# Optimization experiments

Hardware: AMD Instinct MI355X
Metric: run time of the kernel (lower is better)

## Reference

```python
import jax, jax.numpy as jnp
import numpy as np

B, T, F, H = 64, 128, 1024, 1024
FORGET_BIAS = 1.0  # TF BasicLSTMCell default


def setup_inputs() -> dict:
    key = jax.random.key(0)
    k1, k2 = jax.random.split(key, 2)
    x = jax.random.normal(k1, (B, T, F), dtype=jnp.float32)
    # single fused kernel weight [(F+H), 4H], TF gate order: i, j, f, o
    W = jax.random.uniform(k2, (F + H, 4 * H), dtype=jnp.float32, minval=-0.1, maxval=0.1)
    b = jnp.zeros((4 * H,), dtype=jnp.float32)
    return {"x": x, "W": W, "b": b}


def reference(x, W, b):
    # BasicLSTMCell unrolled over time (return_last=False, return_seq_2d=False)
    batch, n_steps, n_feat = x.shape
    n_hidden = W.shape[0] - n_feat

    def step(carry, xt):
        c, h = carry
        z = jnp.concatenate([xt, h], axis=1) @ W + b  # [B, 4H]
        i, j, f, o = jnp.split(z, 4, axis=1)
        c_new = c * jax.nn.sigmoid(f + FORGET_BIAS) + jax.nn.sigmoid(i) * jnp.tanh(j)
        h_new = jnp.tanh(c_new) * jax.nn.sigmoid(o)
        return (c_new, h_new), h_new

    c0 = jnp.zeros((batch, n_hidden), x.dtype)
    h0 = jnp.zeros((batch, n_hidden), x.dtype)
    _, hs = jax.lax.scan(step, (c0, h0), jnp.swapaxes(x, 0, 1))  # [T, B, H]
    return jnp.swapaxes(hs, 0, 1)  # [B, T, H]
```

## Files before the change

kernel.cpp:

```cpp
#include <hip/hip_runtime.h>
#include <hip/hip_bf16.h>

typedef unsigned short u16;
typedef unsigned int u32;
typedef unsigned long long u64;
typedef __bf16 bf16x8 __attribute__((ext_vector_type(8)));
typedef float f32x4 __attribute__((ext_vector_type(4)));

#define NB 64
#define NT 128
#define NF 1024
#define NH 1024
#define NK 2048
#define NG 4096
#define NBH (NB * NH)

#define FSTR 16

#define W_LDS_BYTES 131072
#define ZSX_BYTES (2 * 2 * 64 * 17 * 4)
#define ZSH_BYTES (2 * 64 * 17 * 4)
#define SMEM_BYTES (W_LDS_BYTES + ZSX_BYTES + ZSH_BYTES + 64)

__device__ __forceinline__ u16 f2bf(float f) {
  unsigned u = __builtin_bit_cast(unsigned, f);
  u = (u + 0x7FFFu + ((u >> 16) & 1u)) >> 16;
  return (u16)u;
}
__device__ __forceinline__ float bf2f(u16 v) {
  unsigned u = ((unsigned)v) << 16;
  return __builtin_bit_cast(float, u);
}

__global__ __launch_bounds__(256) void lstm_cvt_x(const float* __restrict__ x,
                                                  u16* __restrict__ xb) {
  int i = (blockIdx.x * 256 + threadIdx.x) * 4;
  float4 v = *reinterpret_cast<const float4*>(x + i);
  ushort4 o;
  o.x = f2bf(v.x); o.y = f2bf(v.y); o.z = f2bf(v.z); o.w = f2bf(v.w);
  *reinterpret_cast<ushort4*>(xb + i) = o;
}

__global__ __launch_bounds__(256) void lstm_prep_w(const float* __restrict__ W,
                                                   u16* __restrict__ wt_blk) {
  __shared__ float tile[32][33];
  int n0 = blockIdx.x * 32;
  int k0 = blockIdx.y * 32;
  int tc = threadIdx.x & 31;
  int tr = threadIdx.x >> 5;
#pragma unroll
  for (int i = 0; i < 4; ++i) {
    int k = tr + i * 8;
    tile[k][tc] = W[(size_t)(k0 + k) * NG + n0 + tc];
  }
  __syncthreads();
#pragma unroll
  for (int i = 0; i < 4; ++i) {
    int n = n0 + tr + i * 8;
    float wv = tile[tc][tr + i * 8];
    int k = k0 + tc;
    int g = n >> 10, col = n & 1023;
    int b = col >> 2, brow = g * 4 + (col & 3);
    int kh = k >> 10, ch = (k & 1023) >> 5;
    int slot = (k >> 3) & 3, elem = k & 7;
    size_t base = (size_t)b * 65536 + (size_t)(kh * 32 + ch) * 512
                + (size_t)(slot * 16 + brow) * 8 + elem;
    u16 hi = f2bf(wv);
    wt_blk[base] = hi;
    wt_blk[base + 32768] = f2bf(wv - bf2f(hi));
  }
}

__device__ __forceinline__ void mfma_pass(const u16* __restrict__ a0, size_t rstride,
                                          const u16* __restrict__ Wl, int khalf,
                                          int kq, int lane, f32x4 acc[4]) {
  bf16x8 pf[4], qf[4];
#pragma unroll
  for (int i = 0; i < 4; ++i)
    pf[i] = *reinterpret_cast<const bf16x8*>(a0 + (size_t)i * 16 * rstride);
#pragma unroll
  for (int cc = 0; cc < 8; ++cc) {
    if (cc < 7) {
#pragma unroll
      for (int i = 0; i < 4; ++i)
        qf[i] = *reinterpret_cast<const bf16x8*>(a0 + (size_t)i * 16 * rstride + (cc + 1) * 32);
    }
    const int ch = kq * 8 + cc;
    const bf16x8 wh = *reinterpret_cast<const bf16x8*>(
        Wl + (size_t)(khalf * 32 + ch) * 512 + lane * 8);
    const bf16x8 wl2 = *reinterpret_cast<const bf16x8*>(
        Wl + (size_t)(64 + khalf * 32 + ch) * 512 + lane * 8);
#pragma unroll
    for (int i = 0; i < 4; ++i)
      acc[i] = __builtin_amdgcn_mfma_f32_16x16x32_bf16(pf[i], wh, acc[i], 0, 0, 0);
#pragma unroll
    for (int i = 0; i < 4; ++i)
      acc[i] = __builtin_amdgcn_mfma_f32_16x16x32_bf16(pf[i], wl2, acc[i], 0, 0, 0);
#pragma unroll
    for (int i = 0; i < 4; ++i) pf[i] = qf[i];
  }
}

__global__ __launch_bounds__(512) void lstm_persist(
    const u16* __restrict__ xb, u16* __restrict__ hseq,
    const u16* __restrict__ wt_blk, const float* __restrict__ bias,
    float* __restrict__ out, u32* __restrict__ flags,
    float* __restrict__ zo) {
  extern __shared__ char smem[];
  u16* Wl = (u16*)smem;
  float (*zsx)[2][64][17] = (float(*)[2][64][17])(smem + W_LDS_BYTES);
  float (*zsh)[64][17] = (float(*)[64][17])(smem + W_LDS_BYTES + ZSX_BYTES);
  volatile u32* hsflag = (volatile u32*)(smem + W_LDS_BYTES + ZSX_BYTES + ZSH_BYTES);

  const int b = blockIdx.x;
  const int tid = threadIdx.x;
  const int lane = tid & 63;
  const int w = tid >> 6;
  const bool is_x = (w < 4);
  const int kq = w & 3;

  {
    const u16* src = wt_blk + (size_t)b * 65536;
#pragma unroll
    for (int it = 0; it < 16; ++it) {
      uint4 v = *reinterpret_cast<const uint4*>(src + (size_t)it * 4096 + tid * 8);
      *reinterpret_cast<uint4*>(Wl + (size_t)it * 4096 + tid * 8) = v;
    }
  }
  for (int i = tid; i < 2 * 64 * 17; i += 512) ((float*)zsh)[i] = 0.f;
  if (tid == 0) hsflag[0] = 0u;

  const int arow = lane & 15;
  const int kfr = 8 * (lane >> 4);
  const int kbase = kq * 256 + kfr;
  const int zn = lane & 15;
  const int mg = (lane >> 4) * 4;

  const int prow = tid >> 1;
  const int pc = (tid & 1) * 2;
  const int gc0 = b * 4 + pc;
  float bz[2][4];
  float creg[2] = {0.f, 0.f};
  if (tid < 128) {
#pragma unroll
    for (int j = 0; j < 2; ++j) {
      bz[j][0] = bias[gc0 + j];
      bz[j][1] = bias[NH + gc0 + j];
      bz[j][2] = bias[2 * NH + gc0 + j];
      bz[j][3] = bias[3 * NH + gc0 + j];
    }
  }
  __syncthreads();

  {
    f32x4 acc[4] = {};
    if (is_x) {
      const u16* a0 = xb + ((size_t)arow * NT + 0) * NF + kbase;
      mfma_pass(a0, (size_t)NT * NF, Wl, 0, kq, lane, acc);
      if (w < 2) {
#pragma unroll
        for (int i = 0; i < 4; ++i)
#pragma unroll
          for (int r = 0; r < 4; ++r) zsx[0][w][i * 16 + mg + r][zn] = acc[i][r];
      }
    }
    __syncthreads();
    if (is_x && w >= 2) {
#pragma unroll
      for (int i = 0; i < 4; ++i)
#pragma unroll
        for (int r = 0; r < 4; ++r) zsx[0][w - 2][i * 16 + mg + r][zn] += acc[i][r];
    }
    __syncthreads();
  }

#pragma unroll 1
  for (int t = 0; t < NT; ++t) {
    const int cb = t & 1;
    const int nb = (t + 1) & 1;
    f32x4 acc[4] = {};

    if (is_x) {
      if (t < NT - 1) {
        const u16* a0 = xb + ((size_t)arow * NT + (t + 1)) * NF + kbase;
        mfma_pass(a0, (size_t)NT * NF, Wl, 0, kq, lane, acc);
      }
    } else {
      if (t > 0) {
        const u32* fp = flags + ((size_t)t * 256 + kq * 64 + lane) * FSTR;
        u32 v = __hip_atomic_load(fp, __ATOMIC_RELAXED, __HIP_MEMORY_SCOPE_AGENT);
        while (!__all(v != 0)) {
          __builtin_amdgcn_s_sleep(1);
          v = __hip_atomic_load(fp, __ATOMIC_RELAXED, __HIP_MEMORY_SCOPE_AGENT);
        }

        const u64* hb = reinterpret_cast<const u64*>(hseq) + (size_t)t * (256 * 64);
        const int sbase = kq * 64 + 2 * (lane >> 4);
        u64 plo[4], phi[4], qlo[4], qhi[4];
#pragma unroll
        for (int i = 0; i < 4; ++i) {
          plo[i] = hb[(size_t)sbase * 64 + arow + 16 * i];
          phi[i] = hb[(size_t)(sbase + 1) * 64 + arow + 16 * i];
        }
        __builtin_amdgcn_s_setprio(1);
#pragma unroll
        for (int cc = 0; cc < 8; ++cc) {
          if (cc < 7) {
            const int s = sbase + (cc + 1) * 8;
#pragma unroll
            for (int i = 0; i < 4; ++i) {
              qlo[i] = hb[(size_t)s * 64 + arow + 16 * i];
              qhi[i] = hb[(size_t)(s + 1) * 64 + arow + 16 * i];
            }
          }
          const int ch = kq * 8 + cc;
          const bf16x8 wh = *reinterpret_cast<const bf16x8*>(
              Wl + (size_t)(32 + ch) * 512 + lane * 8);
          const bf16x8 wlo = *reinterpret_cast<const bf16x8*>(
              Wl + (size_t)(96 + ch) * 512 + lane * 8);
#pragma unroll
          for (int i = 0; i < 4; ++i) {
            union HU { u64 q[2]; bf16x8 f; } u;
            u.q[0] = plo[i];
            u.q[1] = phi[i];
            acc[i] = __builtin_amdgcn_mfma_f32_16x16x32_bf16(u.f, wh, acc[i], 0, 0, 0);
            acc[i] = __builtin_amdgcn_mfma_f32_16x16x32_bf16(u.f, wlo, acc[i], 0, 0, 0);
          }
#pragma unroll
          for (int i = 0; i < 4; ++i) { plo[i] = qlo[i]; phi[i] = qhi[i]; }
        }
        __builtin_amdgcn_s_setprio(0);
      }
    }

    if (is_x) {
      if (w < 2 && t < NT - 1) {
#pragma unroll
        for (int i = 0; i < 4; ++i)
#pragma unroll
          for (int r = 0; r < 4; ++r) zsx[nb][w][i * 16 + mg + r][zn] = acc[i][r];
      }
    } else {
      if (w < 6 && t > 0) {
#pragma unroll
        for (int i = 0; i < 4; ++i)
#pragma unroll
          for (int r = 0; r < 4; ++r) zsh[w - 4][i * 16 + mg + r][zn] = acc[i][r];
      }
    }
    __syncthreads();
    if (is_x) {
      if (w >= 2 && t < NT - 1) {
#pragma unroll
        for (int i = 0; i < 4; ++i)
#pragma unroll
          for (int r = 0; r < 4; ++r) zsx[nb][w - 2][i * 16 + mg + r][zn] += acc[i][r];
      }
    } else {
      if (w >= 6 && t > 0) {
#pragma unroll
        for (int i = 0; i < 4; ++i)
#pragma unroll
          for (int r = 0; r < 4; ++r) zsh[w - 6][i * 16 + mg + r][zn] += acc[i][r];
      }
    }
    __syncthreads();

    if (tid < 128) {
      float hn[2];
#pragma unroll
      for (int jj = 0; jj < 2; ++jj) {
        const int col = pc + jj;
        const float zi = zsx[cb][0][prow][col]      + zsx[cb][1][prow][col]      + zsh[0][prow][col]      + zsh[1][prow][col]      + bz[jj][0];
        const float zj = zsx[cb][0][prow][4 + col]  + zsx[cb][1][prow][4 + col]  + zsh[0][prow][4 + col]  + zsh[1][prow][4 + col]  + bz[jj][1];
        const float zf = zsx[cb][0][prow][8 + col]  + zsx[cb][1][prow][8 + col]  + zsh[0][prow][8 + col]  + zsh[1][prow][8 + col]  + bz[jj][2];
        const float zo4 = zsx[cb][0][prow][12 + col] + zsx[cb][1][prow][12 + col] + zsh[0][prow][12 + col] + zsh[1][prow][12 + col] + bz[jj][3];
        const float si = 1.f / (1.f + __expf(-zi));
        const float tj = tanhf(zj);
        const float sf = 1.f / (1.f + __expf(-(zf + 1.0f)));
        const float so = 1.f / (1.f + __expf(-zo4));
        const float cn = creg[jj] * sf + si * tj;
        hn[jj] = tanhf(cn) * so;
        creg[jj] = cn;
      }
      if (t < NT - 1) {
        u32 hv = (u32)f2bf(hn[0]) | ((u32)f2bf(hn[1]) << 16);
        u32* hp = reinterpret_cast<u32*>(hseq)
                + ((size_t)(t + 1) * 256 + b) * 128 + prow * 2 + (pc >> 1);
        __hip_atomic_store(hp, hv, __ATOMIC_RELAXED, __HIP_MEMORY_SCOPE_AGENT);
        asm volatile("s_waitcnt vmcnt(0)" ::: "memory");
        if (tid == 64) hsflag[0] = (u32)(t + 1);
        if (tid == 0) {
          while (hsflag[0] != (u32)(t + 1)) {}
          __hip_atomic_store(&flags[((size_t)(t + 1) * 256 + b) * FSTR], 1u,
                             __ATOMIC_RELAXED, __HIP_MEMORY_SCOPE_AGENT);
        }
      }
#pragma unroll
      for (int jj = 0; jj < 2; ++jj) {
        __hip_atomic_store(
            reinterpret_cast<u32*>(zo + ((size_t)t * NH + gc0 + jj) * NB + prow),
            __builtin_bit_cast(u32, hn[jj]),
            __ATOMIC_RELAXED, __HIP_MEMORY_SCOPE_AGENT);
      }
    }
  }

  __syncthreads();
  asm volatile("s_waitcnt vmcnt(0)" ::: "memory");
  if (tid == 0)
    __hip_atomic_store(&flags[(size_t)b * FSTR], 1u, __ATOMIC_RELAXED,
                       __HIP_MEMORY_SCOPE_AGENT);
  if (w == 0) {
    bool ok;
    do {
      u32 v0 = __hip_atomic_load(flags + (size_t)(lane * 4 + 0) * FSTR, __ATOMIC_RELAXED, __HIP_MEMORY_SCOPE_AGENT);
      u32 v1 = __hip_atomic_load(flags + (size_t)(lane * 4 + 1) * FSTR, __ATOMIC_RELAXED, __HIP_MEMORY_SCOPE_AGENT);
      u32 v2 = __hip_atomic_load(flags + (size_t)(lane * 4 + 2) * FSTR, __ATOMIC_RELAXED, __HIP_MEMORY_SCOPE_AGENT);
      u32 v3 = __hip_atomic_load(flags + (size_t)(lane * 4 + 3) * FSTR, __ATOMIC_RELAXED, __HIP_MEMORY_SCOPE_AGENT);
      ok = ((v0 & v1 & v2 & v3) == 1u);
      if (!__all(ok)) __builtin_amdgcn_s_sleep(1);
    } while (!__all(ok));
  }
  __syncthreads();

  {
    const int ts = b >> 1;
    const int r0 = (b & 1) * 32;
    float* T = (float*)smem;
#pragma unroll 4
    for (int it = 0; it < 16; ++it) {
      int flat = it * 512 + tid;
      int c = flat >> 3;
      int q = flat & 7;
      const u64* p = reinterpret_cast<const u64*>(
          zo + ((size_t)ts * NH + c) * NB + r0 + q * 4);
      u64 lo = __hip_atomic_load(p + 0, __ATOMIC_RELAXED, __HIP_MEMORY_SCOPE_AGENT);
      u64 hi = __hip_atomic_load(p + 1, __ATOMIC_RELAXED, __HIP_MEMORY_SCOPE_AGENT);
      T[(q * 4 + 0) * 1028 + c] = __builtin_bit_cast(float, (u32)lo);
      T[(q * 4 + 1) * 1028 + c] = __builtin_bit_cast(float, (u32)(lo >> 32));
      T[(q * 4 + 2) * 1028 + c] = __builtin_bit_cast(float, (u32)hi);
      T[(q * 4 + 3) * 1028 + c] = __builtin_bit_cast(float, (u32)(hi >> 32));
    }
    __syncthreads();
#pragma unroll 4
    for (int it = 0; it < 16; ++it) {
      int flat = it * 512 + tid;
      int r = flat >> 8;
      int c4 = flat & 255;
      float4 v;
      v.x = T[r * 1028 + c4 * 4 + 0];
      v.y = T[r * 1028 + c4 * 4 + 1];
      v.z = T[r * 1028 + c4 * 4 + 2];
      v.w = T[r * 1028 + c4 * 4 + 3];
      *reinterpret_cast<float4*>(
          out + ((size_t)(r0 + r) * NT + ts) * NH + c4 * 4) = v;
    }
  }
}

extern "C" void kernel_launch(void* const* d_in, const int* in_sizes, int n_in,
                              void* d_out, int out_size, void* d_ws, size_t ws_size,
                              hipStream_t stream) {
  const float* x = (const float*)d_in[0];
  const float* W = (const float*)d_in[1];
  const float* bias = (const float*)d_in[2];
  float* out = (float*)d_out;

  char* ws = (char*)d_ws;
  u16* xb = (u16*)(ws);
  u16* wt_blk = (u16*)(ws + 16777216);
  u16* hseq = (u16*)(ws + 50331648);
  u32* flags = (u32*)(ws + 67108864);
  float* zo = (float*)(ws + 69206016);

  hipMemsetAsync(hseq, 0, 256 * 512, stream);
  hipMemsetAsync(flags, 0, (size_t)NT * 256 * FSTR * 4, stream);

  lstm_cvt_x<<<(NB * NT * NF) / (256 * 4), 256, 0, stream>>>(x, xb);
  lstm_prep_w<<<dim3(NG / 32, NK / 32), 256, 0, stream>>>(W, wt_blk);

  hipFuncSetAttribute((const void*)lstm_persist,
                      hipFuncAttributeMaxDynamicSharedMemorySize, SMEM_BYTES);

  void* args[] = {(void*)&xb, (void*)&hseq, (void*)&wt_blk, (void*)&bias,
                  (void*)&out, (void*)&flags, (void*)&zo};
  hipLaunchCooperativeKernel((void*)lstm_persist, dim3(256), dim3(512), args,
                             SMEM_BYTES, stream);
}
```

Before: 1.038 ms.

## Replace per-step block barriers with LDS flag-based warp specialization

Replaces the two __syncthreads per timestep with fine-grained LDS counters using release/acquire spin-waits. X-projection waves now run up to two steps ahead of the recurrent waves, and the pointwise work moves onto two of the h waves. The aim is to take the x-side GEMM off the critical serial path and remove block-wide barrier stalls. In exchange it adds spin-waiting in LDS, and there is a risk of ordering bugs in the double-buffered zsx reuse.

```diff
diff --git a/kernel.cpp b/kernel.cpp
--- a/kernel.cpp
+++ b/kernel.cpp
@@ -20,7 +20,18 @@
 #define W_LDS_BYTES 131072
 #define ZSX_BYTES (2 * 2 * 64 * 17 * 4)
 #define ZSH_BYTES (2 * 64 * 17 * 4)
-#define SMEM_BYTES (W_LDS_BYTES + ZSX_BYTES + ZSH_BYTES + 64)
+#define ST_BYTES 64
+#define SMEM_BYTES (W_LDS_BYTES + ZSX_BYTES + ZSH_BYTES + ST_BYTES)
+
+__device__ __forceinline__ void st_rel(u32* p, u32 v) {
+  __hip_atomic_store(p, v, __ATOMIC_RELEASE, __HIP_MEMORY_SCOPE_WORKGROUP);
+}
+__device__ __forceinline__ u32 ld_acq(u32* p) {
+  return __hip_atomic_load(p, __ATOMIC_ACQUIRE, __HIP_MEMORY_SCOPE_WORKGROUP);
+}
+__device__ __forceinline__ void spin_ge(u32* p, u32 v) {
+  while (ld_acq(p) < v) {}
+}
 
 __device__ __forceinline__ u16 f2bf(float f) {
   unsigned u = __builtin_bit_cast(unsigned, f);
@@ -110,14 +121,15 @@
   u16* Wl = (u16*)smem;
   float (*zsx)[2][64][17] = (float(*)[2][64][17])(smem + W_LDS_BYTES);
   float (*zsh)[64][17] = (float(*)[64][17])(smem + W_LDS_BYTES + ZSX_BYTES);
-  volatile u32* hsflag = (volatile u32*)(smem + W_LDS_BYTES + ZSX_BYTES + ZSH_BYTES);
+  u32* st = (u32*)(smem + W_LDS_BYTES + ZSX_BYTES + ZSH_BYTES);
 
   const int b = blockIdx.x;
   const int tid = threadIdx.x;
   const int lane = tid & 63;
-  const int w = tid >> 6;
-  const bool is_x = (w < 4);
-  const int kq = w & 3;
+  const int wv_ = tid >> 6;
+  const bool is_x = (wv_ < 4);
+  const int kq = wv_ & 3;
+  const int hq = wv_ - 4;
 
   {
     const u16* src = wt_blk + (size_t)b * 65536;
@@ -128,7 +140,7 @@
     }
   }
   for (int i = tid; i < 2 * 64 * 17; i += 512) ((float*)zsh)[i] = 0.f;
-  if (tid == 0) hsflag[0] = 0u;
+  if (tid < 16) st[tid] = 0u;
 
   const int arow = lane & 15;
   const int kfr = 8 * (lane >> 4);
@@ -136,12 +148,13 @@
   const int zn = lane & 15;
   const int mg = (lane >> 4) * 4;
 
-  const int prow = tid >> 1;
-  const int pc = (tid & 1) * 2;
+  const int idx = hq * 64 + lane;
+  const int prow = (idx & 127) >> 1;
+  const int pc = (idx & 1) * 2;
   const int gc0 = b * 4 + pc;
   float bz[2][4];
   float creg[2] = {0.f, 0.f};
-  if (tid < 128) {
+  if (!is_x && hq < 2) {
 #pragma unroll
     for (int j = 0; j < 2; ++j) {
       bz[j][0] = bias[gc0 + j];
@@ -152,40 +165,36 @@
   }
   __syncthreads();
 
-  {
-    f32x4 acc[4] = {};
-    if (is_x) {
-      const u16* a0 = xb + ((size_t)arow * NT + 0) * NF + kbase;
+  if (is_x) {
+#pragma unroll 1
+    for (int t = 0; t < NT; ++t) {
+      if (t >= 2) {
+        spin_ge(&st[8], (u32)(t - 1));
+        spin_ge(&st[9], (u32)(t - 1));
+      }
+      f32x4 acc[4] = {};
+      const u16* a0 = xb + ((size_t)arow * NT + t) * NF + kbase;
       mfma_pass(a0, (size_t)NT * NF, Wl, 0, kq, lane, acc);
-      if (w < 2) {
+      const int buf = t & 1;
+      if (kq < 2) {
 #pragma unroll
         for (int i = 0; i < 4; ++i)
 #pragma unroll
-          for (int r = 0; r < 4; ++r) zsx[0][w][i * 16 + mg + r][zn] = acc[i][r];
+          for (int r = 0; r < 4; ++r) zsx[buf][kq][i * 16 + mg + r][zn] = acc[i][r];
+        st_rel(&st[kq], (u32)(t + 1));
+      } else {
+        spin_ge(&st[kq - 2], (u32)(t + 1));
+#pragma unroll
+        for (int i = 0; i < 4; ++i)
+#pragma unroll
+          for (int r = 0; r < 4; ++r) zsx[buf][kq - 2][i * 16 + mg + r][zn] += acc[i][r];
+        st_rel(&st[kq], (u32)(t + 1));
       }
     }
-    __syncthreads();
-    if (is_x && w >= 2) {
-#pragma unroll
-      for (int i = 0; i < 4; ++i)
-#pragma unroll
-        for (int r = 0; r < 4; ++r) zsx[0][w - 2][i * 16 + mg + r][zn] += acc[i][r];
-    }
-    __syncthreads();
-  }
-
+  } else {
 #pragma unroll 1
-  for (int t = 0; t < NT; ++t) {
-    const int cb = t & 1;
-    const int nb = (t + 1) & 1;
-    f32x4 acc[4] = {};
-
-    if (is_x) {
-      if (t < NT - 1) {
-        const u16* a0 = xb + ((size_t)arow * NT + (t + 1)) * NF + kbase;
-        mfma_pass(a0, (size_t)NT * NF, Wl, 0, kq, lane, acc);
-      }
-    } else {
+    for (int t = 0; t < NT; ++t) {
+      f32x4 acc[4] = {};
       if (t > 0) {
         const u32* fp = flags + ((size_t)t * 256 + kq * 64 + lane) * FSTR;
         u32 v = __hip_atomic_load(fp, __ATOMIC_RELAXED, __HIP_MEMORY_SCOPE_AGENT);
@@ -193,7 +202,6 @@
           __builtin_amdgcn_s_sleep(1);
           v = __hip_atomic_load(fp, __ATOMIC_RELAXED, __HIP_MEMORY_SCOPE_AGENT);
         }
-
         const u64* hb = reinterpret_cast<const u64*>(hseq) + (size_t)t * (256 * 64);
         const int sbase = kq * 64 + 2 * (lane >> 4);
         u64 plo[4], phi[4], qlo[4], qhi[4];
@@ -231,77 +239,68 @@
         }
         __builtin_amdgcn_s_setprio(0);
       }
-    }
-
-    if (is_x) {
-      if (w < 2 && t < NT - 1) {
-#pragma unroll
-        for (int i = 0; i < 4; ++i)
-#pragma unroll
-          for (int r = 0; r < 4; ++r) zsx[nb][w][i * 16 + mg + r][zn] = acc[i][r];
-      }
-    } else {
-      if (w < 6 && t > 0) {
-#pragma unroll
-        for (int i = 0; i < 4; ++i)
-#pragma unroll
-          for (int r = 0; r < 4; ++r) zsh[w - 4][i * 16 + mg + r][zn] = acc[i][r];
-      }
-    }
-    __syncthreads();
-    if (is_x) {
-      if (w >= 2 && t < NT - 1) {
-#pragma unroll
-        for (int i = 0; i < 4; ++i)
-#pragma unroll
-          for (int r = 0; r < 4; ++r) zsx[nb][w - 2][i * 16 + mg + r][zn] += acc[i][r];
-      }
-    } else {
-      if (w >= 6 && t > 0) {
-#pragma unroll
-        for (int i = 0; i < 4; ++i)
-#pragma unroll
-          for (int r = 0; r < 4; ++r) zsh[w - 6][i * 16 + mg + r][zn] += acc[i][r];
-      }
-    }
-    __syncthreads();
-
-    if (tid < 128) {
-      float hn[2];
-#pragma unroll
-      for (int jj = 0; jj < 2; ++jj) {
-        const int col = pc + jj;
-        const float zi = zsx[cb][0][prow][col]      + zsx[cb][1][prow][col]      + zsh[0][prow][col]      + zsh[1][prow][col]      + bz[jj][0];
-        const float zj = zsx[cb][0][prow][4 + col]  + zsx[cb][1][prow][4 + col]  + zsh[0][prow][4 + col]  + zsh[1][prow][4 + col]  + bz[jj][1];
-        const float zf = zsx[cb][0][prow][8 + col]  + zsx[cb][1][prow][8 + col]  + zsh[0][prow][8 + col]  + zsh[1][prow][8 + col]  + bz[jj][2];
-        const float zo4 = zsx[cb][0][prow][12 + col] + zsx[cb][1][prow][12 + col] + zsh[0][prow][12 + col] + zsh[1][prow][12 + col] + bz[jj][3];
-        const float si = 1.f / (1.f + __expf(-zi));
-        const float tj = tanhf(zj);
-        const float sf = 1.f / (1.f + __expf(-(zf + 1.0f)));
-        const float so = 1.f / (1.f + __expf(-zo4));
-        const float cn = creg[jj] * sf + si * tj;
-        hn[jj] = tanhf(cn) * so;
-        creg[jj] = cn;
-      }
-      if (t < NT - 1) {
-        u32 hv = (u32)f2bf(hn[0]) | ((u32)f2bf(hn[1]) << 16);
-        u32* hp = reinterpret_cast<u32*>(hseq)
-                + ((size_t)(t + 1) * 256 + b) * 128 + prow * 2 + (pc >> 1);
-        __hip_atomic_store(hp, hv, __ATOMIC_RELAXED, __HIP_MEMORY_SCOPE_AGENT);
-        asm volatile("s_waitcnt vmcnt(0)" ::: "memory");
-        if (tid == 64) hsflag[0] = (u32)(t + 1);
-        if (tid == 0) {
-          while (hsflag[0] != (u32)(t + 1)) {}
-          __hip_atomic_store(&flags[((size_t)(t + 1) * 256 + b) * FSTR], 1u,
-                             __ATOMIC_RELAXED, __HIP_MEMORY_SCOPE_AGENT);
-        }
-      }
-#pragma unroll
-      for (int jj = 0; jj < 2; ++jj) {
-        __hip_atomic_store(
-            reinterpret_cast<u32*>(zo + ((size_t)t * NH + gc0 + jj) * NB + prow),
-            __builtin_bit_cast(u32, hn[jj]),
-            __ATOMIC_RELAXED, __HIP_MEMORY_SCOPE_AGENT);
+
+      if (hq < 2) {
+        spin_ge(&st[8 + (1 - hq)], (u32)t);
+        if (t > 0) {
+#pragma unroll
+          for (int i = 0; i < 4; ++i)
+#pragma unroll
+            for (int r = 0; r < 4; ++r) zsh[hq][i * 16 + mg + r][zn] = acc[i][r];
+        }
+        st_rel(&st[4 + hq], (u32)(t + 1));
+
+        spin_ge(&st[6], (u32)(t + 1));
+        spin_ge(&st[7], (u32)(t + 1));
+        spin_ge(&st[2], (u32)(t + 1));
+        spin_ge(&st[3], (u32)(t + 1));
+        const int cb = t & 1;
+        float hn[2];
+#pragma unroll
+        for (int jj = 0; jj < 2; ++jj) {
+          const int col = pc + jj;
+          const float zi = zsx[cb][0][prow][col]      + zsx[cb][1][prow][col]      + zsh[0][prow][col]      + zsh[1][prow][col]      + bz[jj][0];
+          const float zj = zsx[cb][0][prow][4 + col]  + zsx[cb][1][prow][4 + col]  + zsh[0][prow][4 + col]  + zsh[1][prow][4 + col]  + bz[jj][1];
+          const float zf = zsx[cb][0][prow][8 + col]  + zsx[cb][1][prow][8 + col]  + zsh[0][prow][8 + col]  + zsh[1][prow][8 + col]  + bz[jj][2];
+          const float zo4 = zsx[cb][0][prow][12 + col] + zsx[cb][1][prow][12 + col] + zsh[0][prow][12 + col] + zsh[1][prow][12 + col] + bz[jj][3];
+          const float si = 1.f / (1.f + __expf(-zi));
+          const float tj = tanhf(zj);
+          const float sf = 1.f / (1.f + __expf(-(zf + 1.0f)));
+          const float so = 1.f / (1.f + __expf(-zo4));
+          const float cn = creg[jj] * sf + si * tj;
+          hn[jj] = tanhf(cn) * so;
+          creg[jj] = cn;
+        }
+        if (t < NT - 1) {
+          u32 hv = (u32)f2bf(hn[0]) | ((u32)f2bf(hn[1]) << 16);
+          u32* hp = reinterpret_cast<u32*>(hseq)
+                  + ((size_t)(t + 1) * 256 + b) * 128 + prow * 2 + (pc >> 1);
+          __hip_atomic_store(hp, hv, __ATOMIC_RELAXED, __HIP_MEMORY_SCOPE_AGENT);
+          asm volatile("s_waitcnt vmcnt(0)" ::: "memory");
+        }
+        st_rel(&st[8 + hq], (u32)(t + 1));
+        if (hq == 0 && t < NT - 1) {
+          spin_ge(&st[9], (u32)(t + 1));
+          if (lane == 0)
+            __hip_atomic_store(&flags[((size_t)(t + 1) * 256 + b) * FSTR], 1u,
+                               __ATOMIC_RELAXED, __HIP_MEMORY_SCOPE_AGENT);
+        }
+#pragma unroll
+        for (int jj = 0; jj < 2; ++jj) {
+          __hip_atomic_store(
+              reinterpret_cast<u32*>(zo + ((size_t)t * NH + gc0 + jj) * NB + prow),
+              __builtin_bit_cast(u32, hn[jj]),
+              __ATOMIC_RELAXED, __HIP_MEMORY_SCOPE_AGENT);
+        }
+      } else {
+        spin_ge(&st[4 + (hq - 2)], (u32)(t + 1));
+        if (t > 0) {
+#pragma unroll
+          for (int i = 0; i < 4; ++i)
+#pragma unroll
+            for (int r = 0; r < 4; ++r) zsh[hq - 2][i * 16 + mg + r][zn] += acc[i][r];
+        }
+        st_rel(&st[4 + hq], (u32)(t + 1));
       }
     }
   }
@@ -311,7 +310,7 @@
   if (tid == 0)
     __hip_atomic_store(&flags[(size_t)b * FSTR], 1u, __ATOMIC_RELAXED,
                        __HIP_MEMORY_SCOPE_AGENT);
-  if (w == 0) {
+  if (wv_ == 0) {
     bool ok;
     do {
       u32 v0 = __hip_atomic_load(flags + (size_t)(lane * 4 + 0) * FSTR, __ATOMIC_RELAXED, __HIP_MEMORY_SCOPE_AGENT);
```

New measurement: 1.263 ms. +21.6%, slower.

## Use per-wave step flags, fast tanh, and block-major h staging layout

Applied to the files above, without the earlier changes.

Each of the two pointwise waves now publishes its own readiness flag for the next timestep, and consumers poll both flags. This removes the intra-block LDS handshake and the serial spin by thread 0 on the critical recurrent path. tanhf is replaced with an exp-based formula, which shortens the gate math on that path but loses some accuracy and may overflow to NaN-free saturation only approximately. The staged output is written in a block-major layout with 64-bit stores and read back directly in the final transpose, which drops the LDS transpose pass.

```diff
diff --git a/kernel.cpp b/kernel.cpp
--- a/kernel.cpp
+++ b/kernel.cpp
@@ -30,6 +30,10 @@
 __device__ __forceinline__ float bf2f(u16 v) {
   unsigned u = ((unsigned)v) << 16;
   return __builtin_bit_cast(float, u);
+}
+__device__ __forceinline__ float ftanh(float x) {
+  float e = __expf(2.f * x);
+  return 1.f - 2.f / (e + 1.f);
 }
 
 __global__ __launch_bounds__(256) void lstm_cvt_x(const float* __restrict__ x,
@@ -110,7 +114,6 @@
   u16* Wl = (u16*)smem;
   float (*zsx)[2][64][17] = (float(*)[2][64][17])(smem + W_LDS_BYTES);
   float (*zsh)[64][17] = (float(*)[64][17])(smem + W_LDS_BYTES + ZSX_BYTES);
-  volatile u32* hsflag = (volatile u32*)(smem + W_LDS_BYTES + ZSX_BYTES + ZSH_BYTES);
 
   const int b = blockIdx.x;
   const int tid = threadIdx.x;
@@ -128,7 +131,6 @@
     }
   }
   for (int i = tid; i < 2 * 64 * 17; i += 512) ((float*)zsh)[i] = 0.f;
-  if (tid == 0) hsflag[0] = 0u;
 
   const int arow = lane & 15;
   const int kfr = 8 * (lane >> 4);
@@ -187,13 +189,14 @@
       }
     } else {
       if (t > 0) {
-        const u32* fp = flags + ((size_t)t * 256 + kq * 64 + lane) * FSTR;
-        u32 v = __hip_atomic_load(fp, __ATOMIC_RELAXED, __HIP_MEMORY_SCOPE_AGENT);
-        while (!__all(v != 0)) {
+        const u32* fp = flags + ((size_t)t * 256 + kq * 64 + lane) * 2 * FSTR;
+        u32 v0 = __hip_atomic_load(fp, __ATOMIC_RELAXED, __HIP_MEMORY_SCOPE_AGENT);
+        u32 v1 = __hip_atomic_load(fp + FSTR, __ATOMIC_RELAXED, __HIP_MEMORY_SCOPE_AGENT);
+        while (!__all((v0 & v1) != 0)) {
           __builtin_amdgcn_s_sleep(1);
-          v = __hip_atomic_load(fp, __ATOMIC_RELAXED, __HIP_MEMORY_SCOPE_AGENT);
+          v0 = __hip_atomic_load(fp, __ATOMIC_RELAXED, __HIP_MEMORY_SCOPE_AGENT);
+          v1 = __hip_atomic_load(fp + FSTR, __ATOMIC_RELAXED, __HIP_MEMORY_SCOPE_AGENT);
         }
-
         const u64* hb = reinterpret_cast<const u64*>(hseq) + (size_t)t * (256 * 64);
         const int sbase = kq * 64 + 2 * (lane >> 4);
         u64 plo[4], phi[4], qlo[4], qhi[4];
@@ -276,11 +279,11 @@
         const float zf = zsx[cb][0][prow][8 + col]  + zsx[cb][1][prow][8 + col]  + zsh[0][prow][8 + col]  + zsh[1][prow][8 + col]  + bz[jj][2];
         const float zo4 = zsx[cb][0][prow][12 + col] + zsx[cb][1][prow][12 + col] + zsh[0][prow][12 + col] + zsh[1][prow][12 + col] + bz[jj][3];
         const float si = 1.f / (1.f + __expf(-zi));
-        const float tj = tanhf(zj);
+        const float tj = ftanh(zj);
         const float sf = 1.f / (1.f + __expf(-(zf + 1.0f)));
         const float so = 1.f / (1.f + __expf(-zo4));
         const float cn = creg[jj] * sf + si * tj;
-        hn[jj] = tanhf(cn) * so;
+        hn[jj] = ftanh(cn) * so;
         creg[jj] = cn;
       }
       if (t < NT - 1) {
@@ -289,19 +292,16 @@
                 + ((size_t)(t + 1) * 256 + b) * 128 + prow * 2 + (pc >> 1);
         __hip_atomic_store(hp, hv, __ATOMIC_RELAXED, __HIP_MEMORY_SCOPE_AGENT);
         asm volatile("s_waitcnt vmcnt(0)" ::: "memory");
-        if (tid == 64) hsflag[0] = (u32)(t + 1);
-        if (tid == 0) {
-          while (hsflag[0] != (u32)(t + 1)) {}
-          __hip_atomic_store(&flags[((size_t)(t + 1) * 256 + b) * FSTR], 1u,
-                             __ATOMIC_RELAXED, __HIP_MEMORY_SCOPE_AGENT);
-        }
-      }
-#pragma unroll
-      for (int jj = 0; jj < 2; ++jj) {
+        if (lane == 0)
+          __hip_atomic_store(
+              &flags[(((size_t)(t + 1) * 256 + b) * 2 + w) * FSTR], 1u,
+              __ATOMIC_RELAXED, __HIP_MEMORY_SCOPE_AGENT);
+      }
+      {
+        double d = __builtin_bit_cast(double, *reinterpret_cast<u64*>(hn));
         __hip_atomic_store(
-            reinterpret_cast<u32*>(zo + ((size_t)t * NH + gc0 + jj) * NB + prow),
-            __builtin_bit_cast(u32, hn[jj]),
-            __ATOMIC_RELAXED, __HIP_MEMORY_SCOPE_AGENT);
+            reinterpret_cast<u64*>(zo + ((size_t)t * 256 + b) * 256 + prow * 4 + pc),
+            __builtin_bit_cast(u64, d), __ATOMIC_RELAXED, __HIP_MEMORY_SCOPE_AGENT);
       }
     }
   }
@@ -309,15 +309,15 @@
   __syncthreads();
   asm volatile("s_waitcnt vmcnt(0)" ::: "memory");
   if (tid == 0)
-    __hip_atomic_store(&flags[(size_t)b * FSTR], 1u, __ATOMIC_RELAXED,
+    __hip_atomic_store(&flags[(size_t)b * 2 * FSTR], 1u, __ATOMIC_RELAXED,
                        __HIP_MEMORY_SCOPE_AGENT);
   if (w == 0) {
     bool ok;
     do {
-      u32 v0 = __hip_atomic_load(flags + (size_t)(lane * 4 + 0) * FSTR, __ATOMIC_RELAXED, __HIP_MEMORY_SCOPE_AGENT);
-      u32 v1 = __hip_atomic_load(flags + (size_t)(lane * 4 + 1) * FSTR, __ATOMIC_RELAXED, __HIP_MEMORY_SCOPE_AGENT);
-      u32 v2 = __hip_atomic_load(flags + (size_t)(lane * 4 + 2) * FSTR, __ATOMIC_RELAXED, __HIP_MEMORY_SCOPE_AGENT);
-      u32 v3 = __hip_atomic_load(flags + (size_t)(lane * 4 + 3) * FSTR, __ATOMIC_RELAXED, __HIP_MEMORY_SCOPE_AGENT);
+      u32 v0 = __hip_atomic_load(flags + (size_t)(lane * 4 + 0) * 2 * FSTR, __ATOMIC_RELAXED, __HIP_MEMORY_SCOPE_AGENT);
+      u32 v1 = __hip_atomic_load(flags + (size_t)(lane * 4 + 1) * 2 * FSTR, __ATOMIC_RELAXED, __HIP_MEMORY_SCOPE_AGENT);
+      u32 v2 = __hip_atomic_load(flags + (size_t)(lane * 4 + 2) * 2 * FSTR, __ATOMIC_RELAXED, __HIP_MEMORY_SCOPE_AGENT);
+      u32 v3 = __hip_atomic_load(flags + (size_t)(lane * 4 + 3) * 2 * FSTR, __ATOMIC_RELAXED, __HIP_MEMORY_SCOPE_AGENT);
       ok = ((v0 & v1 & v2 & v3) == 1u);
       if (!__all(ok)) __builtin_amdgcn_s_sleep(1);
     } while (!__all(ok));
@@ -327,32 +327,20 @@
   {
     const int ts = b >> 1;
     const int r0 = (b & 1) * 32;
-    float* T = (float*)smem;
-#pragma unroll 4
-    for (int it = 0; it < 16; ++it) {
-      int flat = it * 512 + tid;
-      int c = flat >> 3;
-      int q = flat & 7;
-      const u64* p = reinterpret_cast<const u64*>(
-          zo + ((size_t)ts * NH + c) * NB + r0 + q * 4);
-      u64 lo = __hip_atomic_load(p + 0, __ATOMIC_RELAXED, __HIP_MEMORY_SCOPE_AGENT);
-      u64 hi = __hip_atomic_load(p + 1, __ATOMIC_RELAXED, __HIP_MEMORY_SCOPE_AGENT);
-      T[(q * 4 + 0) * 1028 + c] = __builtin_bit_cast(float, (u32)lo);
-      T[(q * 4 + 1) * 1028 + c] = __builtin_bit_cast(float, (u32)(lo >> 32));
-      T[(q * 4 + 2) * 1028 + c] = __builtin_bit_cast(float, (u32)hi);
-      T[(q * 4 + 3) * 1028 + c] = __builtin_bit_cast(float, (u32)(hi >> 32));
-    }
-    __syncthreads();
 #pragma unroll 4
     for (int it = 0; it < 16; ++it) {
       int flat = it * 512 + tid;
       int r = flat >> 8;
       int c4 = flat & 255;
+      const u64* p = reinterpret_cast<const u64*>(
+          zo + ((size_t)ts * 256 + c4) * 256 + (size_t)(r0 + r) * 4);
+      u64 lo = __hip_atomic_load(p + 0, __ATOMIC_RELAXED, __HIP_MEMORY_SCOPE_AGENT);
+      u64 hi = __hip_atomic_load(p + 1, __ATOMIC_RELAXED, __HIP_MEMORY_SCOPE_AGENT);
       float4 v;
-      v.x = T[r * 1028 + c4 * 4 + 0];
-      v.y = T[r * 1028 + c4 * 4 + 1];
-      v.z = T[r * 1028 + c4 * 4 + 2];
-      v.w = T[r * 1028 + c4 * 4 + 3];
+      v.x = __builtin_bit_cast(float, (u32)lo);
+      v.y = __builtin_bit_cast(float, (u32)(lo >> 32));
+      v.z = __builtin_bit_cast(float, (u32)hi);
+      v.w = __builtin_bit_cast(float, (u32)(hi >> 32));
       *reinterpret_cast<float4*>(
           out + ((size_t)(r0 + r) * NT + ts) * NH + c4 * 4) = v;
     }
@@ -372,10 +360,10 @@
   u16* wt_blk = (u16*)(ws + 16777216);
   u16* hseq = (u16*)(ws + 50331648);
   u32* flags = (u32*)(ws + 67108864);
-  float* zo = (float*)(ws + 69206016);
+  float* zo = (float*)(ws + 71303168);
 
   hipMemsetAsync(hseq, 0, 256 * 512, stream);
-  hipMemsetAsync(flags, 0, (size_t)NT * 256 * FSTR * 4, stream);
+  hipMemsetAsync(flags, 0, (size_t)NT * 512 * FSTR * 4, stream);
 
   lstm_cvt_x<<<(NB * NT * NF) / (256 * 4), 256, 0, stream>>>(x, xb);
   lstm_prep_w<<<dim3(NG / 32, NK / 32), 256, 0, stream>>>(W, wt_blk);
```

Result: slower. 1.281 ms (+23.3%).

## Use fast exp-based tanh and store outputs in block-major layout

Applied to the files above, without the earlier changes.

Replaces tanhf with an exp-based tanh approximation in the recurrent gate math, shortening the per-step critical path. Changes the staging layout of h outputs so each thread writes an 8-byte packed store and the final copy reads 16-byte chunks straight into the output. This removes the LDS transpose and a barrier from the epilogue. The fast tanh can lose accuracy or overflow to inf for large inputs, though 1-2/(inf+1) still evaluates to 1.

```diff
diff --git a/kernel.cpp b/kernel.cpp
--- a/kernel.cpp
+++ b/kernel.cpp
@@ -30,6 +30,10 @@
 __device__ __forceinline__ float bf2f(u16 v) {
   unsigned u = ((unsigned)v) << 16;
   return __builtin_bit_cast(float, u);
+}
+__device__ __forceinline__ float ftanh(float x) {
+  float e = __expf(2.f * x);
+  return 1.f - 2.f / (e + 1.f);
 }
 
 __global__ __launch_bounds__(256) void lstm_cvt_x(const float* __restrict__ x,
@@ -276,11 +280,11 @@
         const float zf = zsx[cb][0][prow][8 + col]  + zsx[cb][1][prow][8 + col]  + zsh[0][prow][8 + col]  + zsh[1][prow][8 + col]  + bz[jj][2];
         const float zo4 = zsx[cb][0][prow][12 + col] + zsx[cb][1][prow][12 + col] + zsh[0][prow][12 + col] + zsh[1][prow][12 + col] + bz[jj][3];
         const float si = 1.f / (1.f + __expf(-zi));
-        const float tj = tanhf(zj);
+        const float tj = ftanh(zj);
         const float sf = 1.f / (1.f + __expf(-(zf + 1.0f)));
         const float so = 1.f / (1.f + __expf(-zo4));
         const float cn = creg[jj] * sf + si * tj;
-        hn[jj] = tanhf(cn) * so;
+        hn[jj] = ftanh(cn) * so;
         creg[jj] = cn;
       }
       if (t < NT - 1) {
@@ -296,12 +300,12 @@
                              __ATOMIC_RELAXED, __HIP_MEMORY_SCOPE_AGENT);
         }
       }
-#pragma unroll
-      for (int jj = 0; jj < 2; ++jj) {
+      {
+        u64 dv;
+        memcpy(&dv, hn, 8);
         __hip_atomic_store(
-            reinterpret_cast<u32*>(zo + ((size_t)t * NH + gc0 + jj) * NB + prow),
-            __builtin_bit_cast(u32, hn[jj]),
-            __ATOMIC_RELAXED, __HIP_MEMORY_SCOPE_AGENT);
+            reinterpret_cast<u64*>(zo + ((size_t)t * 256 + b) * 256 + prow * 4 + pc),
+            dv, __ATOMIC_RELAXED, __HIP_MEMORY_SCOPE_AGENT);
       }
     }
   }
@@ -327,32 +331,20 @@
   {
     const int ts = b >> 1;
     const int r0 = (b & 1) * 32;
-    float* T = (float*)smem;
-#pragma unroll 4
-    for (int it = 0; it < 16; ++it) {
-      int flat = it * 512 + tid;
-      int c = flat >> 3;
-      int q = flat & 7;
-      const u64* p = reinterpret_cast<const u64*>(
-          zo + ((size_t)ts * NH + c) * NB + r0 + q * 4);
-      u64 lo = __hip_atomic_load(p + 0, __ATOMIC_RELAXED, __HIP_MEMORY_SCOPE_AGENT);
-      u64 hi = __hip_atomic_load(p + 1, __ATOMIC_RELAXED, __HIP_MEMORY_SCOPE_AGENT);
-      T[(q * 4 + 0) * 1028 + c] = __builtin_bit_cast(float, (u32)lo);
-      T[(q * 4 + 1) * 1028 + c] = __builtin_bit_cast(float, (u32)(lo >> 32));
-      T[(q * 4 + 2) * 1028 + c] = __builtin_bit_cast(float, (u32)hi);
-      T[(q * 4 + 3) * 1028 + c] = __builtin_bit_cast(float, (u32)(hi >> 32));
-    }
-    __syncthreads();
 #pragma unroll 4
     for (int it = 0; it < 16; ++it) {
       int flat = it * 512 + tid;
       int r = flat >> 8;
       int c4 = flat & 255;
+      const u64* p = reinterpret_cast<const u64*>(
+          zo + ((size_t)ts * 256 + c4) * 256 + (size_t)(r0 + r) * 4);
+      u64 lo = __hip_atomic_load(p + 0, __ATOMIC_RELAXED, __HIP_MEMORY_SCOPE_AGENT);
+      u64 hi = __hip_atomic_load(p + 1, __ATOMIC_RELAXED, __HIP_MEMORY_SCOPE_AGENT);
       float4 v;
-      v.x = T[r * 1028 + c4 * 4 + 0];
-      v.y = T[r * 1028 + c4 * 4 + 1];
-      v.z = T[r * 1028 + c4 * 4 + 2];
-      v.w = T[r * 1028 + c4 * 4 + 3];
+      v.x = __builtin_bit_cast(float, (u32)lo);
+      v.y = __builtin_bit_cast(float, (u32)(lo >> 32));
+      v.z = __builtin_bit_cast(float, (u32)hi);
+      v.w = __builtin_bit_cast(float, (u32)(hi >> 32));
       *reinterpret_cast<float4*>(
           out + ((size_t)(r0 + r) * NT + ts) * NH + c4 * 4) = v;
     }
```

Result: slower. 1.097 ms (+5.6%).
